# Kernel tuning notes

Hardware: AMD Instinct MI355X
Metric: run time of the kernel (lower is better)

The kernel has to match this reference:

```python
import jax, jax.numpy as jnp
import numpy as np
from jax import lax

# SLAYER SRMALPHA neuron / simulation constants (from init params)
THETA = 10.0      # spike threshold
TAU_SR = 10.0     # synaptic (PSP) alpha-kernel time constant
TAU_REF = 1.0     # refractory alpha-kernel time constant
SCALE_REF = 2.0   # refractory kernel scale (x theta)
TS = 1.0          # simulation timestep


def _alpha_filter(x, tau):
    """Causal convolution of x[T, ...] with the SLAYER alpha kernel
    k[n] = (n*TS/tau) * exp(1 - n*TS/tau)  (note k[0] = 0),
    implemented as a 2-state linear recurrence (exact, O(T)).
    k[n] = c * n * a**n with a = exp(-TS/tau), c = e*TS/tau.
    """
    a = jnp.asarray(np.exp(-TS / tau), x.dtype)
    c = jnp.asarray(np.e * TS / tau, x.dtype)

    def step(carry, xn):
        p, q = carry              # p[n-1] = sum a^{n-1-m} x[m]; q[n-1] = sum (n-1-m) a^{n-1-m} x[m]
        q = a * q + a * p         # q[n]
        p = a * p + xn            # p[n]
        return (p, q), c * q      # y[n] = c*q[n]  (x[n] has weight k[0]=0)

    z = jnp.zeros_like(x[0])
    _, y = lax.scan(step, (z, z), x)
    return y


def _spike_with_refractory(u):
    """SLAYER spike: threshold membrane potential u[T, B, O]; each emitted
    spike injects the refractory alpha kernel -scaleRef*theta*(t/tauRef)*exp(1-t/tauRef)
    into the future membrane potential. Same 2-state alpha recurrence, but the
    filtered signal is the (data-dependent) spike train -> sequential scan.
    """
    a = jnp.asarray(np.exp(-TS / TAU_REF), u.dtype)
    c = jnp.asarray(-SCALE_REF * THETA * np.e * TS / TAU_REF, u.dtype)

    def step(carry, un):
        p, q = carry
        q = a * q + a * p                       # refractory trace of past spikes
        s = (un + c * q >= THETA).astype(un.dtype)
        p = a * p + s
        return (p, q), s

    z = jnp.zeros_like(u[0])
    _, s = lax.scan(step, (z, z), u)
    return s


def setup_inputs() -> dict:
    key = jax.random.key(0)
    k1, k2 = jax.random.split(key)
    B, CIN, COUT, T = 32, 1024, 1024, 500
    spike_input = (jax.random.uniform(k1, (B, CIN, 1, 1, T)) < 0.05).astype(jnp.float32)
    W = jax.random.normal(k2, (COUT, CIN), dtype=jnp.float32) * (1.0 / np.sqrt(CIN))
    return {"spike_input": spike_input, "W": W}


def reference(spike_input, W):
    B, C, _, _, T = spike_input.shape
    O = W.shape[0]
    x = spike_input.reshape(B, C, T).transpose(2, 0, 1)   # [T, B, C]
    psp = _alpha_filter(x, TAU_SR)                        # temporal PSP filter
    u = jnp.einsum('tbc,oc->tbo', psp, W)                 # slayer.dense = 1x1 conv = GEMM
    s = _spike_with_refractory(u)                         # threshold + refractory
    return s.transpose(1, 2, 0).reshape(B, O, 1, 1, T)
```

## Files before the change

### kernel.cpp

```cpp
#include <hip/hip_runtime.h>
#include <cstddef>
#include <cstdint>

#define T_DIM 500
#define B_DIM 32
#define C_DIM 1024
#define O_DIM 1024
#define M_DIM (T_DIM * B_DIM)
#define MP_DIM 16128
#define BO_DIM (B_DIM * O_DIM)

typedef __attribute__((ext_vector_type(4))) int i32x4;

static __device__ __forceinline__ ushort f2bf(float x) {
  unsigned u = __float_as_uint(x);
  return (ushort)((u + 0x7FFF + ((u >> 16) & 1)) >> 16);
}
static __device__ __forceinline__ float bf2f(ushort u) {
  return __uint_as_float(((unsigned)u) << 16);
}

static __device__ __forceinline__ i32x4 ldsri(const char* p) {
  i32x4 d;
  asm volatile("ds_read_b128 %0, %1"
               : "=v"(d)
               : "v"((unsigned)(uintptr_t)(const __attribute__((address_space(3))) char*)p));
  return d;
}

__global__ __launch_bounds__(256) void k_transpose(const float* __restrict__ x,
                                                   char* __restrict__ xt) {
  __shared__ float tile[32][33];
  const int b  = blockIdx.z;
  const int t0 = blockIdx.x * 32;
  const int c0 = blockIdx.y * 32;
  const int tx = threadIdx.x;
  const int ty = threadIdx.y;

  const int t = t0 + tx;
  if (t < T_DIM) {
#pragma unroll
    for (int r = 0; r < 4; ++r) {
      const int c = c0 + ty + r * 8;
      tile[ty + r * 8][tx] = x[((size_t)b * C_DIM + c) * T_DIM + t];
    }
  }
  __syncthreads();
#pragma unroll
  for (int r = 0; r < 4; ++r) {
    const int tt = t0 + ty + r * 8;
    if (tt < T_DIM) {
      xt[((size_t)tt * B_DIM + b) * C_DIM + c0 + tx] = (char)tile[tx][ty + r * 8];
    }
  }
}

__global__ __launch_bounds__(256) void k_quant_w(const float4* __restrict__ W,
                                                 char* __restrict__ Wq) {
  const int i = blockIdx.x * 256 + threadIdx.x;
  const float4 w = W[i];
  char4 q;
  q.x = (char)max(-127, min(127, (int)rintf(w.x * 512.0f)));
  q.y = (char)max(-127, min(127, (int)rintf(w.y * 512.0f)));
  q.z = (char)max(-127, min(127, (int)rintf(w.z * 512.0f)));
  q.w = (char)max(-127, min(127, (int)rintf(w.w * 512.0f)));
  *(char4*)&Wq[(size_t)i * 4] = q;
}

__global__ __launch_bounds__(256, 2) void k_gemm_i8(const char* __restrict__ A,
                                                    const char* __restrict__ Bw,
                                                    ushort* __restrict__ C) {
  __shared__ char lds[73728];

  const int tid  = threadIdx.x;
  const int wid  = tid >> 6;
  const int lane = tid & 63;

  const int orig = blockIdx.x;
  const int swz  = (orig & 7) * 63 + (orig >> 3);
  const int row0 = (swz >> 3) * 256;
  const int col0 = (swz & 7) * 128;

  const int wm = wid >> 1;
  const int wn = wid & 1;

  i32x4 acc[8][4] = {};

  const int sk = (((tid & 3) ^ ((tid >> 3) & 3)) * 16);
  const char* Ab = A  + (size_t)(row0 + (tid >> 2)) * C_DIM + sk;
  const char* Bb = Bw + (size_t)(col0 + (tid >> 2)) * C_DIM + sk;

  const int fr  = lane & 15;
  const int g4  = lane >> 4;
  const int fsw = (g4 ^ ((fr >> 1) & 3)) * 16;
  const int aoff = (wm * 128 + fr) * 64 + fsw;
  const int boff = 16384 + (wn * 64 + fr) * 64 + fsw;

#define STG(K0S, SB)                                                              \
  do {                                                                            \
    _Pragma("unroll")                                                             \
    for (int L = 0; L < 4; ++L)                                                   \
      __builtin_amdgcn_global_load_lds(                                           \
          (const __attribute__((address_space(1))) void*)(Ab + (size_t)L * 64 * C_DIM + (K0S)), \
          (__attribute__((address_space(3))) void*)&lds[(SB) + L * 4096 + tid * 16], 16, 0, 0);  \
    _Pragma("unroll")                                                             \
    for (int L = 0; L < 2; ++L)                                                   \
      __builtin_amdgcn_global_load_lds(                                           \
          (const __attribute__((address_space(1))) void*)(Bb + (size_t)L * 64 * C_DIM + (K0S)), \
          (__attribute__((address_space(3))) void*)&lds[(SB) + 16384 + L * 4096 + tid * 16], 16, 0, 0); \
  } while (0)

#define ROW_(i, N)                                                             \
  do {                                                                         \
    asm volatile("s_waitcnt lgkmcnt(" #N ")" ::: "memory");                    \
    __builtin_amdgcn_sched_barrier(0);                                         \
    _Pragma("unroll")                                                          \
    for (int j = 0; j < 4; ++j)                                                \
      asm volatile("v_mfma_i32_16x16x64_i8 %0, %1, %2, %0"                     \
                   : "+v"(acc[i][j]) : "v"(a[i]), "v"(b[j]));                  \
  } while (0)

  STG(0, 0);
  STG(64, 24576);

  int cur = 0;
  int nxt = 49152;

  for (int t = 0; t < 16; ++t) {
    if (t < 15) { asm volatile("s_waitcnt vmcnt(6)" ::: "memory"); }
    else        { asm volatile("s_waitcnt vmcnt(0)" ::: "memory"); }
    __builtin_amdgcn_s_barrier();

    i32x4 a[8], b[4];
#pragma unroll
    for (int j = 0; j < 4; ++j) b[j] = ldsri(&lds[cur + boff + j * 1024]);
#pragma unroll
    for (int i = 0; i < 8; ++i) a[i] = ldsri(&lds[cur + aoff + i * 1024]);

    if (t <= 13) { STG((t + 2) * 64, nxt); }

    __builtin_amdgcn_s_setprio(1);
    ROW_(0, 7); ROW_(1, 6); ROW_(2, 5); ROW_(3, 4);
    ROW_(4, 3); ROW_(5, 2); ROW_(6, 1); ROW_(7, 0);
    __builtin_amdgcn_s_setprio(0);

    cur = (cur == 49152) ? 0 : cur + 24576;
    nxt = (nxt == 49152) ? 0 : nxt + 24576;
  }

  const int crow = (lane >> 4) * 4;
  const int ccol = lane & 15;
#pragma unroll
  for (int i = 0; i < 8; ++i)
#pragma unroll
    for (int j = 0; j < 4; ++j) {
      ushort* cp = C + (size_t)(row0 + wm * 128 + i * 16 + crow) * O_DIM
                     + (col0 + wn * 64 + j * 16 + ccol);
#pragma unroll
      for (int r = 0; r < 4; ++r)
        cp[(size_t)r * O_DIM] = f2bf((float)acc[i][j][r] * (1.0f / 512.0f));
    }
#undef STG
#undef ROW_
}

__global__ __launch_bounds__(64) void k_scan(const ushort* __restrict__ v,
                                             float* __restrict__ out) {
  const int g = blockIdx.x * 64 + threadIdx.x;

  const float a1 = 0.90483741803595952f;
  const float c1 = 0.27182818284590452f;
  const float a2 = 0.36787944117144233f;
  const float c2 = -54.365636569180905f;

  float p1 = 0.f, q1 = 0.f;
  float p2 = 0.f, q2 = 0.f;

  const ushort* vp = v + g;
  float* op = out + (size_t)g * T_DIM;

  constexpr int D  = 20;
  constexpr int NC = 25;

  ushort b0[D], b1[D], b2[D];
#pragma unroll
  for (int j = 0; j < D; ++j) b0[j] = vp[(size_t)j * BO_DIM];
#pragma unroll
  for (int j = 0; j < D; ++j) b1[j] = vp[(size_t)(D + j) * BO_DIM];
#pragma unroll
  for (int j = 0; j < D; ++j) b2[j] = vp[(size_t)(2 * D + j) * BO_DIM];

#pragma unroll 5
  for (int c = 0; c < NC; ++c) {
    const int cn = (c + 3 < NC) ? (c + 3) : (NC - 1);
    ushort bn[D];
    {
      const size_t base = (size_t)cn * D;
#pragma unroll
      for (int j = 0; j < D; ++j) bn[j] = vp[(base + j) * BO_DIM];
    }

    float rr[D];
#pragma unroll
    for (int j = 0; j < D; ++j) {
      const float vn = bf2f(b0[j]);
      q1 = a1 * q1 + a1 * p1;
      p1 = a1 * p1 + vn;
      const float u = c1 * q1;
      q2 = a2 * q2 + a2 * p2;
      const float s = (u + c2 * q2 >= 10.0f) ? 1.0f : 0.0f;
      p2 = a2 * p2 + s;
      rr[j] = s;
    }

    float* o = op + c * D;
#pragma unroll
    for (int j = 0; j < D; j += 4)
      *(float4*)&o[j] = make_float4(rr[j], rr[j + 1], rr[j + 2], rr[j + 3]);

#pragma unroll
    for (int j = 0; j < D; ++j) { b0[j] = b1[j]; b1[j] = b2[j]; b2[j] = bn[j]; }
  }
}

extern "C" void kernel_launch(void* const* d_in, const int* in_sizes, int n_in,
                              void* d_out, int out_size, void* d_ws, size_t ws_size,
                              hipStream_t stream) {
  const float* x = (const float*)d_in[0];
  const float* W = (const float*)d_in[1];
  float* out = (float*)d_out;

  ushort* v  = (ushort*)d_ws;
  char*   xt = (char*)(v + (size_t)MP_DIM * O_DIM);
  char*   Wq = xt + (size_t)MP_DIM * C_DIM;

  dim3 g0((T_DIM + 31) / 32, C_DIM / 32, B_DIM);
  k_transpose<<<g0, dim3(32, 8), 0, stream>>>(x, xt);

  k_quant_w<<<(O_DIM * C_DIM / 4) / 256, 256, 0, stream>>>((const float4*)W, Wq);

  k_gemm_i8<<<(MP_DIM / 256) * (O_DIM / 128), 256, 0, stream>>>(xt, Wq, v);

  k_scan<<<BO_DIM / 64, 64, 0, stream>>>(v, out);
}
```

Measured before the change: 75.90 us.

## Load GEMM B operand directly into registers, bypassing LDS staging

The int8 GEMM no longer stages the weight (B) tile through LDS. Each wave now loads its B fragments straight from global memory into registers, double-buffered across iterations. Only the A tile still goes through the LDS triple buffer, which shrinks LDS use from 72 KB to 48 KB, and the barrier moves to the end of each iteration. The aim is to cut LDS traffic and LDS footprint. The cost is redundant global/L2 reads of B across the two wm waves and more register pressure.

New measurement: 83.72 us. 10.3% more time.

```diff
diff --git a/kernel.cpp b/kernel.cpp
--- a/kernel.cpp
+++ b/kernel.cpp
@@ -70,7 +70,7 @@
 __global__ __launch_bounds__(256, 2) void k_gemm_i8(const char* __restrict__ A,
                                                     const char* __restrict__ Bw,
                                                     ushort* __restrict__ C) {
-  __shared__ char lds[73728];
+  __shared__ char lds[49152];
 
   const int tid  = threadIdx.x;
   const int wid  = tid >> 6;
@@ -87,65 +87,76 @@
   i32x4 acc[8][4] = {};
 
   const int sk = (((tid & 3) ^ ((tid >> 3) & 3)) * 16);
-  const char* Ab = A  + (size_t)(row0 + (tid >> 2)) * C_DIM + sk;
-  const char* Bb = Bw + (size_t)(col0 + (tid >> 2)) * C_DIM + sk;
+  const char* Ab = A + (size_t)(row0 + (tid >> 2)) * C_DIM + sk;
 
   const int fr  = lane & 15;
   const int g4  = lane >> 4;
   const int fsw = (g4 ^ ((fr >> 1) & 3)) * 16;
   const int aoff = (wm * 128 + fr) * 64 + fsw;
-  const int boff = 16384 + (wn * 64 + fr) * 64 + fsw;
-
-#define STG(K0S, SB)                                                              \
-  do {                                                                            \
-    _Pragma("unroll")                                                             \
-    for (int L = 0; L < 4; ++L)                                                   \
-      __builtin_amdgcn_global_load_lds(                                           \
-          (const __attribute__((address_space(1))) void*)(Ab + (size_t)L * 64 * C_DIM + (K0S)), \
-          (__attribute__((address_space(3))) void*)&lds[(SB) + L * 4096 + tid * 16], 16, 0, 0);  \
-    _Pragma("unroll")                                                             \
-    for (int L = 0; L < 2; ++L)                                                   \
-      __builtin_amdgcn_global_load_lds(                                           \
-          (const __attribute__((address_space(1))) void*)(Bb + (size_t)L * 64 * C_DIM + (K0S)), \
-          (__attribute__((address_space(3))) void*)&lds[(SB) + 16384 + L * 4096 + tid * 16], 16, 0, 0); \
+
+  const char* Bg0 = Bw + (size_t)(col0 + wn * 64 + fr) * C_DIM + g4 * 16;
+  const char* Bg1 = Bg0 + 16 * C_DIM;
+  const char* Bg2 = Bg0 + 32 * C_DIM;
+  const char* Bg3 = Bg0 + 48 * C_DIM;
+
+#define STG_A(K0S, SB)                                                            \
+  _Pragma("unroll")                                                               \
+  for (int L = 0; L < 4; ++L)                                                     \
+    __builtin_amdgcn_global_load_lds(                                             \
+        (const __attribute__((address_space(1))) void*)(Ab + (size_t)L * 64 * C_DIM + (K0S)), \
+        (__attribute__((address_space(3))) void*)&lds[(SB) + L * 4096 + tid * 16], 16, 0, 0)
+
+#define LD_B(dst, T)                                                           \
+  do {                                                                         \
+    dst[0] = *(const i32x4*)(Bg0 + (size_t)(T) * 64);                          \
+    dst[1] = *(const i32x4*)(Bg1 + (size_t)(T) * 64);                          \
+    dst[2] = *(const i32x4*)(Bg2 + (size_t)(T) * 64);                          \
+    dst[3] = *(const i32x4*)(Bg3 + (size_t)(T) * 64);                          \
   } while (0)
 
-#define ROW_(i, N)                                                             \
+#define ROW_(i, N, bv)                                                         \
   do {                                                                         \
     asm volatile("s_waitcnt lgkmcnt(" #N ")" ::: "memory");                    \
     __builtin_amdgcn_sched_barrier(0);                                         \
     _Pragma("unroll")                                                          \
     for (int j = 0; j < 4; ++j)                                                \
       asm volatile("v_mfma_i32_16x16x64_i8 %0, %1, %2, %0"                     \
-                   : "+v"(acc[i][j]) : "v"(a[i]), "v"(b[j]));                  \
+                   : "+v"(acc[i][j]) : "v"(a[i]), "v"(bv[j]));                 \
   } while (0)
 
-  STG(0, 0);
-  STG(64, 24576);
+#define ITER(t, BUSE, BLOAD)                                                   \
+  do {                                                                         \
+    i32x4 a[8];                                                                \
+    _Pragma("unroll")                                                          \
+    for (int i = 0; i < 8; ++i) a[i] = ldsri(&lds[cur + aoff + i * 1024]);     \
+    if ((t) < 15) { LD_B(BLOAD, (t) + 1); }                                    \
+    if ((t) <= 13) { STG_A(((t) + 2) * 64, nxt); }                             \
+    __builtin_amdgcn_s_setprio(1);                                             \
+    ROW_(0, 7, BUSE); ROW_(1, 6, BUSE); ROW_(2, 5, BUSE); ROW_(3, 4, BUSE);    \
+    ROW_(4, 3, BUSE); ROW_(5, 2, BUSE); ROW_(6, 1, BUSE); ROW_(7, 0, BUSE);    \
+    __builtin_amdgcn_s_setprio(0);                                             \
+    if ((t) < 14)       { asm volatile("s_waitcnt vmcnt(6)" ::: "memory");     \
+                          __builtin_amdgcn_s_barrier(); }                      \
+    else if ((t) == 14) { asm volatile("s_waitcnt vmcnt(0)" ::: "memory");     \
+                          __builtin_amdgcn_s_barrier(); }                      \
+    cur = (cur == 32768) ? 0 : cur + 16384;                                    \
+    nxt = (nxt == 32768) ? 0 : nxt + 16384;                                    \
+  } while (0)
+
+  i32x4 bA[4], bB[4];
+
+  LD_B(bA, 0);
+  STG_A(0, 0);
+  STG_A(64, 16384);
+  asm volatile("s_waitcnt vmcnt(6)" ::: "memory");
+  __builtin_amdgcn_s_barrier();
 
   int cur = 0;
-  int nxt = 49152;
-
-  for (int t = 0; t < 16; ++t) {
-    if (t < 15) { asm volatile("s_waitcnt vmcnt(6)" ::: "memory"); }
-    else        { asm volatile("s_waitcnt vmcnt(0)" ::: "memory"); }
-    __builtin_amdgcn_s_barrier();
-
-    i32x4 a[8], b[4];
-#pragma unroll
-    for (int j = 0; j < 4; ++j) b[j] = ldsri(&lds[cur + boff + j * 1024]);
-#pragma unroll
-    for (int i = 0; i < 8; ++i) a[i] = ldsri(&lds[cur + aoff + i * 1024]);
-
-    if (t <= 13) { STG((t + 2) * 64, nxt); }
-
-    __builtin_amdgcn_s_setprio(1);
-    ROW_(0, 7); ROW_(1, 6); ROW_(2, 5); ROW_(3, 4);
-    ROW_(4, 3); ROW_(5, 2); ROW_(6, 1); ROW_(7, 0);
-    __builtin_amdgcn_s_setprio(0);
-
-    cur = (cur == 49152) ? 0 : cur + 24576;
-    nxt = (nxt == 49152) ? 0 : nxt + 24576;
+  int nxt = 32768;
+
+  for (int tt = 0; tt < 8; ++tt) {
+    ITER(2 * tt,     bA, bB);
+    ITER(2 * tt + 1, bB, bA);
   }
 
   const int crow = (lane >> 4) * 4;
@@ -160,8 +171,10 @@
       for (int r = 0; r < 4; ++r)
         cp[(size_t)r * O_DIM] = f2bf((float)acc[i][j][r] * (1.0f / 512.0f));
     }
-#undef STG
+#undef STG_A
+#undef LD_B
 #undef ROW_
+#undef ITER
 }
 
 __global__ __launch_bounds__(64) void k_scan(const ushort* __restrict__ v,
```
